# Optimization experiments

Measured on AMD Instinct MI355X. Metric: run time of the kernel, lower is better.

The kernel has to match this reference:

```python
import jax, jax.numpy as jnp
import numpy as np

N_EMBD = 1024
N_HEAD = 16
HEAD_DIM = N_EMBD // N_HEAD
SEQ = 2048
BATCH = 2
WINDOW = 256
SCALE = 1.0 / np.sqrt(HEAD_DIM)
MASK_VALUE = -10000.0


def setup_inputs() -> dict:
    key = jax.random.key(0)
    ks = jax.random.split(key, 5)
    s = 0.02
    return {
        "hidden_states": jax.random.normal(ks[0], (BATCH, SEQ, N_EMBD), dtype=jnp.float32),
        "w_attn": jax.random.normal(ks[1], (N_EMBD, 3 * N_EMBD), dtype=jnp.float32) * s,
        "b_attn": jnp.zeros((3 * N_EMBD,), dtype=jnp.float32),
        "w_proj": jax.random.normal(ks[2], (N_EMBD, N_EMBD), dtype=jnp.float32) * s,
        "b_proj": jnp.zeros((N_EMBD,), dtype=jnp.float32),
    }


def _mask(seq_len):
    # causal AND sliding window: j <= i and j > i - WINDOW
    i = jnp.arange(seq_len)[:, None]
    j = jnp.arange(seq_len)[None, :]
    return (j <= i) & (j > i - WINDOW)  # [T, T] bool


def reference(hidden_states, w_attn, b_attn, w_proj, b_proj):
    B, T, _ = hidden_states.shape
    qkv = hidden_states @ w_attn + b_attn  # [B, T, 3E]
    q, k, v = jnp.split(qkv, 3, axis=-1)
    # [B, H, T, D]
    q = q.reshape(B, T, N_HEAD, HEAD_DIM).transpose(0, 2, 1, 3)
    k = k.reshape(B, T, N_HEAD, HEAD_DIM).transpose(0, 2, 1, 3)
    v = v.reshape(B, T, N_HEAD, HEAD_DIM).transpose(0, 2, 1, 3)

    scores = jnp.einsum("bhqd,bhkd->bhqk", q, k) * SCALE  # [B, H, T, T]
    mask = _mask(T)[None, None]  # [1, 1, T, T]
    scores = jnp.where(mask, scores, MASK_VALUE)
    scores = jnp.clip(scores, -10000.0, 10000.0)
    attn = jax.nn.softmax(scores, axis=-1)
    out = jnp.einsum("bhqk,bhkd->bhqd", attn, v)  # [B, H, T, D]
    out = out.transpose(0, 2, 1, 3).reshape(B, T, N_EMBD)
    return out @ w_proj + b_proj
```

## Files before the change

kernel.cpp:

```cpp
#include <hip/hip_runtime.h>


typedef __bf16 bf16_t;
typedef bf16_t bf16x8 __attribute__((ext_vector_type(8)));
typedef bf16_t bf16x4 __attribute__((ext_vector_type(4)));
typedef float  floatx4 __attribute__((ext_vector_type(4)));

#define SEQ_T   2048
#define NHEAD   16
#define HDIM    64
#define EMB     1024
#define WIN     256
#define SCALE_F 0.125f

__device__ __forceinline__ int detect_bf16(const uint4* __restrict__ det)
{
    const int lane = threadIdx.x & 63;
    const uint4 v = det[lane];
    int c = 0;
    #pragma unroll
    for (int e = 0; e < 4; ++e) {
        const unsigned int ex = ((&v.x)[e] >> 7) & 0xffu;
        c += (ex >= 100u && ex <= 150u) ? 1 : 0;
    }
    #pragma unroll
    for (int m = 32; m >= 1; m >>= 1) c += __shfl_xor(c, m, 64);
    return (c * 2 > 256) ? 1 : 0;
}

__global__ __launch_bounds__(256) void prologue(
    const void* __restrict__ hidden, bf16_t* __restrict__ Hc,
    const void* __restrict__ ba, bf16_t* __restrict__ bba,
    const void* __restrict__ bp, bf16_t* __restrict__ bbp,
    const void* __restrict__ wA, bf16_t* __restrict__ WtA,
    const void* __restrict__ wP, bf16_t* __restrict__ WtP)
{
    __shared__ __align__(16) bf16_t tile[64][68];
    const int f = detect_bf16((const uint4*)hidden);
    const int blk = blockIdx.x;

    if (blk < 4100) {
        if (f) return;
        const float* src;
        bf16_t* dst;
        int base;
        if (blk < 4096)      { src = (const float*)hidden; dst = Hc;  base = blk * 1024; }
        else if (blk < 4099) { src = (const float*)ba;     dst = bba; base = (blk - 4096) * 1024; }
        else                 { src = (const float*)bp;     dst = bbp; base = 0; }
        const int i4 = base + threadIdx.x * 4;
        const float4 x = *(const float4*)(src + i4);
        bf16x4 v;
        v[0] = (bf16_t)x.x; v[1] = (bf16_t)x.y;
        v[2] = (bf16_t)x.z; v[3] = (bf16_t)x.w;
        *(bf16x4*)(dst + i4) = v;
        return;
    }

    int id = blk - 4100;
    const void* W; bf16_t* Wt; int N, bx, by;
    if (id < 768) { W = wA; Wt = WtA; N = 3072; bx = id % 48; by = id / 48; }
    else { id -= 768; W = wP; Wt = WtP; N = 1024; bx = id % 16; by = id / 16; }
    const int K = 1024;
    const int n0 = bx * 64;
    const int k0 = by * 64;
    const int tx = threadIdx.x & 15;
    const int ty = threadIdx.x >> 4;

    #pragma unroll
    for (int r = ty; r < 64; r += 16) {
        bf16x4 v;
        const size_t base = (size_t)(k0 + r) * N + n0 + tx * 4;
        if (f) {
            v = *(const bf16x4*)((const bf16_t*)W + base);
        } else {
            const float4 x = *(const float4*)((const float*)W + base);
            v[0] = (bf16_t)x.x; v[1] = (bf16_t)x.y;
            v[2] = (bf16_t)x.z; v[3] = (bf16_t)x.w;
        }
        *(bf16x4*)&tile[r][tx * 4] = v;
    }
    __syncthreads();
    #pragma unroll
    for (int r = ty; r < 64; r += 16) {
        bf16x4 v;
        v[0] = tile[tx * 4 + 0][r];
        v[1] = tile[tx * 4 + 1][r];
        v[2] = tile[tx * 4 + 2][r];
        v[3] = tile[tx * 4 + 3][r];
        *(bf16x4*)(Wt + (size_t)(n0 + r) * K + k0 + tx * 4) = v;
    }
}

template<int BNt, int BKt>
__global__ __launch_bounds__(256, 2) void gemm_bt_bias(
    const bf16_t* __restrict__ Abf,
    const bf16_t* __restrict__ Aalt,
    const bf16_t* __restrict__ Bt,
    const bf16_t* __restrict__ biasbf,
    const bf16_t* __restrict__ biasalt,
    void* __restrict__ C,
    int M, int N, int K,
    int force_bf16, const uint4* __restrict__ det)
{
    constexpr int BMt = 128;
    constexpr int NF  = BNt / 32;
    constexpr int LPR = BKt / 8;
    constexpr int CM  = LPR - 1;
    constexpr int RPL = 64 / LPR;
    constexpr int SL  = BKt / 32;
    __shared__ __align__(16) bf16_t As[BMt * BKt];
    __shared__ __align__(16) bf16_t Bs[BNt * BKt];

    const int flag = detect_bf16(det);
    const bf16_t* A    = flag ? Abf    : Aalt;
    const bf16_t* bias = flag ? biasbf : biasalt;
    const int obf = force_bf16 | flag;

    const int tid  = threadIdx.x;
    const int wave = tid >> 6;
    const int lane = tid & 63;
    const int quad = lane >> 4;
    const int n16  = lane & 15;
    const int m0 = blockIdx.y * BMt;
    const int n0 = blockIdx.x * BNt;
    const int wm = (wave >> 1) * 64;
    const int wn = (wave & 1) * (BNt / 2);

    floatx4 acc[4][NF] = {};

    const int lr   = lane / LPR;
    const int lc16 = lane % LPR;

    for (int k0 = 0; k0 < K; k0 += BKt) {
        #pragma unroll
        for (int t = 0; t < (BMt / 4) / RPL; ++t) {
            const int row0 = wave * (BMt / 4) + t * RPL;
            const int g = (lc16 ^ ((row0 + lr) & CM)) * 8;
            const bf16_t* ga = A + (size_t)(m0 + row0 + lr) * K + k0 + g;
            __builtin_amdgcn_global_load_lds(
                (const __attribute__((address_space(1))) void*)ga,
                (__attribute__((address_space(3))) void*)(As + row0 * BKt),
                16, 0, 0);
        }
        #pragma unroll
        for (int t = 0; t < (BNt / 4) / RPL; ++t) {
            const int row0 = wave * (BNt / 4) + t * RPL;
            const int g = (lc16 ^ ((row0 + lr) & CM)) * 8;
            const bf16_t* gb = Bt + (size_t)(n0 + row0 + lr) * K + k0 + g;
            __builtin_amdgcn_global_load_lds(
                (const __attribute__((address_space(1))) void*)gb,
                (__attribute__((address_space(3))) void*)(Bs + row0 * BKt),
                16, 0, 0);
        }
        __syncthreads();

        #pragma unroll
        for (int s = 0; s < SL; ++s) {
            const int ch = (((4 * s + quad) ^ (n16 & CM)) * 8);
            const bf16_t* pa = As + (wm + n16) * BKt + ch;
            const bf16_t* pb = Bs + (wn + n16) * BKt + ch;
            bf16x8 af[4], bfr[NF];
            #pragma unroll
            for (int ff = 0; ff < 4; ++ff)
                af[ff] = *(const bf16x8*)(pa + ff * 16 * BKt);
            #pragma unroll
            for (int ff = 0; ff < NF; ++ff)
                bfr[ff] = *(const bf16x8*)(pb + ff * 16 * BKt);
            #pragma unroll
            for (int mf = 0; mf < 4; ++mf)
                #pragma unroll
                for (int nf = 0; nf < NF; ++nf)
                    acc[mf][nf] = __builtin_amdgcn_mfma_f32_16x16x32_bf16(
                        af[mf], bfr[nf], acc[mf][nf], 0, 0, 0);
        }
        __syncthreads();
    }

    const int col   = n0 + wn + n16;
    const int rbase = m0 + wm + quad * 4;
    #pragma unroll
    for (int nf = 0; nf < NF; ++nf) {
        const float bv = (float)bias[col + nf * 16];
        #pragma unroll
        for (int mf = 0; mf < 4; ++mf) {
            #pragma unroll
            for (int r = 0; r < 4; ++r) {
                const size_t idx =
                    (size_t)(rbase + mf * 16 + r) * N + col + nf * 16;
                const float val = acc[mf][nf][r] + bv;
                if (obf) ((bf16_t*)C)[idx] = (bf16_t)val;
                else     ((float*)C)[idx]  = val;
            }
        }
    }
}

#define CW   80
#define NCH  4
#define VT_S 128
#define P_S  104

__device__ __forceinline__ int vt_salt(int d) { return (d ^ (d >> 3)) & 7; }

__global__ __launch_bounds__(256) void attn_mfma(
    const bf16_t* __restrict__ qkv,
    bf16_t* __restrict__ attn_out)
{
    __shared__ __align__(16) bf16_t Ks[CW * 64];
    __shared__ __align__(16) bf16_t Vt[64 * VT_S];
    __shared__ __align__(16) bf16_t Pst[4][16 * P_S];

    const int tid  = threadIdx.x;
    const int wave = tid >> 6;
    const int lane = tid & 63;
    const int quad = lane >> 4;
    const int n16  = lane & 15;

    const int i0 = blockIdx.x * 64;
    const int h  = blockIdx.y;
    const int b  = blockIdx.z;
    const size_t rowbase = (size_t)b * SEQ_T;
    const int kbase  = i0 - 256;
    const int iw     = 16 * wave;
    const int climit = 256 - i0;

    const bf16_t* Qg = qkv + (rowbase + i0 + iw + n16) * (3 * EMB) + h * HDIM;
    bf16x8 qf[2];
    qf[0] = *(const bf16x8*)(Qg + quad * 8);
    qf[1] = *(const bf16x8*)(Qg + 32 + quad * 8);

    for (int i = tid; i < 1024; i += 256) {
        const int d = i >> 4;
        const int k = 80 + (i & 15);
        Vt[d * VT_S + (((k >> 3) ^ vt_salt(d)) << 3) + (k & 7)] = (bf16_t)0.f;
    }
    for (int i = tid; i < 1024; i += 256)
        Pst[i >> 8][((i >> 4) & 15) * P_S + 80 + (i & 15)] = (bf16_t)0.f;

    floatx4 Oac[4] = {};
    float m_run[4], l_run[4];
    #pragma unroll
    for (int rr = 0; rr < 4; ++rr) { m_run[rr] = -3.0e38f; l_run[rr] = 0.f; }

    bf16x8 vreg[3];

    auto loadV = [&](int hc) {
        const int cbase = hc * CW;
        #pragma unroll
        for (int t = 0; t < 3; ++t) {
            const int idx = tid + 256 * t;
            if (idx < 640) {
                const int lc = idx >> 3;
                const int d0 = (idx & 7) * 8;
                int j = kbase + cbase + lc; if (j < 0) j = 0;
                vreg[t] = *(const bf16x8*)(qkv + (rowbase + j) * (3 * EMB)
                                           + 2 * EMB + h * HDIM + d0);
            }
        }
    };
    auto stageK = [&](int hc) {
        const int cbase = hc * CW;
        for (int t = wave; t < 10; t += 4) {
            const int lc0 = t * 8;
            const int lcL = lc0 + (lane >> 3);
            int j = kbase + cbase + lcL; if (j < 0) j = 0;
            const int g = (lane & 7) ^ (lane >> 3);
            const bf16_t* src = qkv + (rowbase + j) * (3 * EMB)
                                + EMB + h * HDIM + g * 8;
            __builtin_amdgcn_global_load_lds(
                (const __attribute__((address_space(1))) void*)src,
                (__attribute__((address_space(3))) void*)(Ks + lc0 * 64),
                16, 0, 0);
        }
    };
    auto writeVt = [&]() {
        #pragma unroll
        for (int t = 0; t < 3; ++t) {
            const int idx = tid + 256 * t;
            if (idx < 640) {
                const int lc = idx >> 3;
                const int d0 = (idx & 7) * 8;
                #pragma unroll
                for (int e = 0; e < 8; ++e) {
                    const int d = d0 + e;
                    Vt[d * VT_S + (((lc >> 3) ^ vt_salt(d)) << 3) + (lc & 7)]
                        = vreg[t][e];
                }
            }
        }
    };

    loadV(0);
    stageK(0);

    for (int hc = 0; hc < NCH; ++hc) {
        const int cbase = hc * CW;

        __syncthreads();
        writeVt();
        __syncthreads();

        if (hc < NCH - 1) loadV(hc + 1);

        floatx4 sc[5];
        __builtin_amdgcn_s_setprio(1);
        #pragma unroll
        for (int tt = 0; tt < 5; ++tt) {
            sc[tt] = (floatx4){0.f, 0.f, 0.f, 0.f};
            #pragma unroll
            for (int s2 = 0; s2 < 2; ++s2) {
                const int lc = 16 * tt + n16;
                const int ch = (4 * s2 + quad) ^ (lc & 7);
                const bf16x8 kf = *(const bf16x8*)(Ks + lc * 64 + ch * 8);
                sc[tt] = __builtin_amdgcn_mfma_f32_16x16x32_bf16(
                    qf[s2], kf, sc[tt], 0, 0, 0);
            }
        }
        __builtin_amdgcn_s_setprio(0);

        #pragma unroll
        for (int tt = 0; tt < 5; ++tt) {
            const int c  = cbase + 16 * tt + n16;
            const int cw = c - iw;
            #pragma unroll
            for (int rr = 0; rr < 4; ++rr) {
                const int r = quad * 4 + rr;
                const bool valid = (cw > r) && (cw <= r + 256) && (c >= climit);
                sc[tt][rr] = valid ? sc[tt][rr] * SCALE_F : -3.0e38f;
            }
        }

        float cm[4];
        #pragma unroll
        for (int rr = 0; rr < 4; ++rr) {
            cm[rr] = -3.0e38f;
            #pragma unroll
            for (int tt = 0; tt < 5; ++tt) cm[rr] = fmaxf(cm[rr], sc[tt][rr]);
            #pragma unroll
            for (int m = 8; m >= 1; m >>= 1)
                cm[rr] = fmaxf(cm[rr], __shfl_xor(cm[rr], m, 64));
        }
        #pragma unroll
        for (int rr = 0; rr < 4; ++rr) {
            const float mnew  = fmaxf(m_run[rr], cm[rr]);
            const float alpha = __expf(m_run[rr] - mnew);
            m_run[rr] = mnew;
            l_run[rr] *= alpha;
            #pragma unroll
            for (int nt = 0; nt < 4; ++nt) Oac[nt][rr] *= alpha;
        }

        float psum[4] = {0.f, 0.f, 0.f, 0.f};
        #pragma unroll
        for (int tt = 0; tt < 5; ++tt) {
            #pragma unroll
            for (int rr = 0; rr < 4; ++rr) {
                const float s = sc[tt][rr];
                const float e = (s > -1.0e38f) ? __expf(s - m_run[rr]) : 0.f;
                psum[rr] += e;
                Pst[wave][(quad * 4 + rr) * P_S + 16 * tt + n16] = (bf16_t)e;
            }
        }
        #pragma unroll
        for (int rr = 0; rr < 4; ++rr) {
            #pragma unroll
            for (int m = 8; m >= 1; m >>= 1)
                psum[rr] += __shfl_xor(psum[rr], m, 64);
            l_run[rr] += psum[rr];
        }

        __syncthreads();

        if (hc < NCH - 1) stageK(hc + 1);

        __builtin_amdgcn_s_setprio(1);
        #pragma unroll
        for (int ks = 0; ks < 3; ++ks) {
            const bf16x8 paf = *(const bf16x8*)(
                &Pst[wave][n16 * P_S + ks * 32 + quad * 8]);
            #pragma unroll
            for (int nt = 0; nt < 4; ++nt) {
                const int d = nt * 16 + n16;
                const int cc = (ks * 4 + quad) ^ vt_salt(d);
                const bf16x8 vbf = *(const bf16x8*)(Vt + d * VT_S + cc * 8);
                Oac[nt] = __builtin_amdgcn_mfma_f32_16x16x32_bf16(
                    paf, vbf, Oac[nt], 0, 0, 0);
            }
        }
        __builtin_amdgcn_s_setprio(0);
    }

    #pragma unroll
    for (int rr = 0; rr < 4; ++rr) {
        const float rden = 1.0f / l_run[rr];
        const size_t row = rowbase + i0 + iw + quad * 4 + rr;
        #pragma unroll
        for (int nt = 0; nt < 4; ++nt) {
            attn_out[row * EMB + h * HDIM + nt * 16 + n16] =
                (bf16_t)(Oac[nt][rr] * rden);
        }
    }
}

extern "C" void kernel_launch(void* const* d_in, const int* in_sizes, int n_in,
                              void* d_out, int out_size, void* d_ws, size_t ws_size,
                              hipStream_t stream)
{
    const void* hidden = d_in[0];
    const void* w_attn = d_in[1];
    const void* b_attn = d_in[2];
    const void* w_proj = d_in[3];
    const void* b_proj = d_in[4];

    char* ws = (char*)d_ws;
    bf16_t* Wt_attn = (bf16_t*)(ws);
    bf16_t* Wt_proj = (bf16_t*)(ws + (6u << 20));
    bf16_t* qkv     = (bf16_t*)(ws + (8u << 20));
    bf16_t* attn_o  = (bf16_t*)(ws + (32u << 20));
    bf16_t* Hc      = (bf16_t*)(ws + (40u << 20));
    bf16_t* bb_attn = (bf16_t*)(ws + (48u << 20));
    bf16_t* bb_proj = (bf16_t*)(ws + (48u << 20) + 8192);

    const uint4* det = (const uint4*)hidden;

    prologue<<<5124, 256, 0, stream>>>(hidden, Hc, b_attn, bb_attn,
                                       b_proj, bb_proj,
                                       w_attn, Wt_attn, w_proj, Wt_proj);

    gemm_bt_bias<192, 128><<<dim3(3072 / 192, 4096 / 128), 256, 0, stream>>>(
        (const bf16_t*)hidden, Hc, Wt_attn,
        (const bf16_t*)b_attn, bb_attn, qkv, 4096, 3072, 1024, 1, det);

    attn_mfma<<<dim3(SEQ_T / 64, NHEAD, 2), 256, 0, stream>>>(qkv, attn_o);

    gemm_bt_bias<64, 128><<<dim3(1024 / 64, 4096 / 128), 256, 0, stream>>>(
        attn_o, attn_o, Wt_proj,
        (const bf16_t*)b_proj, bb_proj, (void*)d_out, 4096, 1024, 1024, 0, det);
}
```

Measured before the change: 161.8 us.

## Add 512-thread 256x192 QKV GEMM with direct-to-LDS loads and phased MFMA

Replaces the QKV projection GEMM with a new kernel that uses 8 waves, a larger 256x192 tile, and a BK of 64. It double-buffers tiles through global_load_lds with an XOR swizzle and spreads the next-tile loads across four MFMA phases. Barriers and setprio interleave memory traffic with compute. The kernel also adds a block-id swizzle for L2 locality. The grid shrinks to 256 blocks, which may underfill the 256 CUs and raises LDS and register pressure in exchange for more reuse per block.

```diff
diff --git a/kernel.cpp b/kernel.cpp
--- a/kernel.cpp
+++ b/kernel.cpp
@@ -88,6 +88,142 @@
         v[2] = tile[tx * 4 + 2][r];
         v[3] = tile[tx * 4 + 3][r];
         *(bf16x4*)(Wt + (size_t)(n0 + r) * K + k0 + tx * 4) = v;
+    }
+}
+
+__global__ __launch_bounds__(512, 2) void gemm_qkv_8p(
+    const bf16_t* __restrict__ Abf,
+    const bf16_t* __restrict__ Aalt,
+    const bf16_t* __restrict__ Bt,
+    const bf16_t* __restrict__ biasbf,
+    const bf16_t* __restrict__ biasalt,
+    void* __restrict__ C,
+    int M, int N, int K,
+    int force_bf16, const uint4* __restrict__ det)
+{
+    constexpr int BMt = 256, BNt = 192, BKt = 64;
+    constexpr int CM  = 7;
+    __shared__ __align__(16) bf16_t As[2][BMt * BKt];
+    __shared__ __align__(16) bf16_t Bs[2][BNt * BKt];
+
+    const int flag = detect_bf16(det);
+    const bf16_t* A    = flag ? Abf    : Aalt;
+    const bf16_t* bias = flag ? biasbf : biasalt;
+    const int obf = force_bf16 | flag;
+
+    const int tid  = threadIdx.x;
+    const int wave = tid >> 6;
+    const int lane = tid & 63;
+    const int quad = lane >> 4;
+    const int n16  = lane & 15;
+
+    const int bid = blockIdx.x + blockIdx.y * gridDim.x;
+    const int swz = (bid & 7) * 32 + (bid >> 3);
+    const int n0  = (swz & 15) * BNt;
+    const int m0  = (swz >> 4) * BMt;
+
+    const int wm = (wave >> 2) * 128;
+    const int wn = (wave & 3) * 48;
+
+    floatx4 acc[8][3] = {};
+
+    const int lr   = lane >> 3;
+    const int lc16 = lane & 7;
+
+    auto stageA = [&](int bsel, int k0) {
+        #pragma unroll
+        for (int t = 0; t < 4; ++t) {
+            const int row0 = wave * 32 + t * 8;
+            const int g = (lc16 ^ ((row0 + lr) & CM)) * 8;
+            const bf16_t* ga = A + (size_t)(m0 + row0 + lr) * K + k0 + g;
+            __builtin_amdgcn_global_load_lds(
+                (const __attribute__((address_space(1))) void*)ga,
+                (__attribute__((address_space(3))) void*)(As[bsel] + row0 * BKt),
+                16, 0, 0);
+        }
+    };
+    auto stageB = [&](int bsel, int k0) {
+        #pragma unroll
+        for (int t = 0; t < 3; ++t) {
+            const int row0 = wave * 24 + t * 8;
+            const int g = (lc16 ^ ((row0 + lr) & CM)) * 8;
+            const bf16_t* gb = Bt + (size_t)(n0 + row0 + lr) * K + k0 + g;
+            __builtin_amdgcn_global_load_lds(
+                (const __attribute__((address_space(1))) void*)gb,
+                (__attribute__((address_space(3))) void*)(Bs[bsel] + row0 * BKt),
+                16, 0, 0);
+        }
+    };
+
+    stageA(0, 0);
+    stageB(0, 0);
+
+    const int NIT = K / BKt;
+    for (int it = 0; it < NIT; ++it) {
+        const int buf = it & 1;
+        __syncthreads();
+
+        const bf16_t* __restrict__ Ab = As[buf];
+        const bf16_t* __restrict__ Bb = Bs[buf];
+
+        bf16x8 bfr[3][2];
+        #pragma unroll
+        for (int nf = 0; nf < 3; ++nf)
+            #pragma unroll
+            for (int ks = 0; ks < 2; ++ks) {
+                const int row = wn + nf * 16 + n16;
+                const int ch  = ((4 * ks + quad) ^ (row & CM)) * 8;
+                bfr[nf][ks] = *(const bf16x8*)(Bb + row * BKt + ch);
+            }
+
+        #pragma unroll
+        for (int ph = 0; ph < 4; ++ph) {
+            bf16x8 af[2][2];
+            #pragma unroll
+            for (int mf2 = 0; mf2 < 2; ++mf2)
+                #pragma unroll
+                for (int ks = 0; ks < 2; ++ks) {
+                    const int row = wm + (ph * 2 + mf2) * 16 + n16;
+                    const int ch  = ((4 * ks + quad) ^ (row & CM)) * 8;
+                    af[mf2][ks] = *(const bf16x8*)(Ab + row * BKt + ch);
+                }
+            if (it + 1 < NIT) {
+                if (ph == 0) stageA(buf ^ 1, (it + 1) * BKt);
+                if (ph == 1) stageB(buf ^ 1, (it + 1) * BKt);
+            }
+            __builtin_amdgcn_s_barrier();
+            __builtin_amdgcn_s_setprio(1);
+            #pragma unroll
+            for (int mf2 = 0; mf2 < 2; ++mf2)
+                #pragma unroll
+                for (int nf = 0; nf < 3; ++nf)
+                    #pragma unroll
+                    for (int ks = 0; ks < 2; ++ks)
+                        acc[ph * 2 + mf2][nf] =
+                            __builtin_amdgcn_mfma_f32_16x16x32_bf16(
+                                af[mf2][ks], bfr[nf][ks],
+                                acc[ph * 2 + mf2][nf], 0, 0, 0);
+            __builtin_amdgcn_s_setprio(0);
+            if (ph < 3) __builtin_amdgcn_s_barrier();
+        }
+    }
+
+    const int col   = n0 + wn + n16;
+    const int rbase = m0 + wm + quad * 4;
+    #pragma unroll
+    for (int nf = 0; nf < 3; ++nf) {
+        const float bv = (float)bias[col + nf * 16];
+        #pragma unroll
+        for (int mf = 0; mf < 8; ++mf) {
+            #pragma unroll
+            for (int r = 0; r < 4; ++r) {
+                const size_t idx =
+                    (size_t)(rbase + mf * 16 + r) * N + col + nf * 16;
+                const float val = acc[mf][nf][r] + bv;
+                if (obf) ((bf16_t*)C)[idx] = (bf16_t)val;
+                else     ((float*)C)[idx]  = val;
+            }
+        }
     }
 }
 
@@ -427,7 +563,7 @@
                                        b_proj, bb_proj,
                                        w_attn, Wt_attn, w_proj, Wt_proj);
 
-    gemm_bt_bias<192, 128><<<dim3(3072 / 192, 4096 / 128), 256, 0, stream>>>(
+    gemm_qkv_8p<<<dim3(16, 16), 512, 0, stream>>>(
         (const bf16_t*)hidden, Hc, Wt_attn,
         (const bf16_t*)b_attn, bb_attn, qkv, 4096, 3072, 1024, 1, det);
 
```

Result: slower. 166.2 us (+2.7%).
